# Kernel tuning notes

Hardware: AMD Instinct MI355X
Metric: run time of the kernel (lower is better)

Reference implementation:

```python
import jax, jax.numpy as jnp
import numpy as np

B, S, D = 4, 1024, 512
E = 16            # num_skills
DH = 4 * D        # expert hidden
DS = 2 * D        # shared expert hidden
TOP_K = 2
TEMP = 0.7
SHARED_SCALE = 0.25
EPS = 1e-5

def layer_norm(x, g, b):
    mu = jnp.mean(x, axis=-1, keepdims=True)
    var = jnp.mean(jnp.square(x - mu), axis=-1, keepdims=True)
    return (x - mu) * jax.lax.rsqrt(var + EPS) * g + b

def setup_inputs() -> dict:
    key = jax.random.key(0)
    ks = jax.random.split(key, 12)
    s = 0.02
    return {
        "x": jax.random.normal(ks[0], (B, S, D), jnp.float32),
        # input LayerNorm
        "ln_in_g": jnp.ones((D,), jnp.float32),
        "ln_in_b": jnp.zeros((D,), jnp.float32),
        # router Linear(D -> E)
        "router_w": jax.random.normal(ks[1], (D, E), jnp.float32) * s,
        "router_b": jnp.zeros((E,), jnp.float32),
        # experts: Linear(D->DH), SiLU, Linear(DH->D), stacked over E
        "ew1": jax.random.normal(ks[2], (E, D, DH), jnp.float32) * s,
        "eb1": jnp.zeros((E, DH), jnp.float32),
        "ew2": jax.random.normal(ks[3], (E, DH, D), jnp.float32) * s,
        "eb2": jnp.zeros((E, D), jnp.float32),
        # shared expert: Linear(D->DS), SiLU, Linear(DS->D), *0.25
        "sw1": jax.random.normal(ks[4], (D, DS), jnp.float32) * s,
        "sb1": jnp.zeros((DS,), jnp.float32),
        "sw2": jax.random.normal(ks[5], (DS, D), jnp.float32) * s,
        "sb2": jnp.zeros((D,), jnp.float32),
        # final ff: LayerNorm, Linear(D->4D), SiLU, Linear(4D->D)
        "ff_ln_g": jnp.ones((D,), jnp.float32),
        "ff_ln_b": jnp.zeros((D,), jnp.float32),
        "ff_w1": jax.random.normal(ks[6], (D, DH), jnp.float32) * s,
        "ff_b1": jnp.zeros((DH,), jnp.float32),
        "ff_w2": jax.random.normal(ks[7], (DH, D), jnp.float32) * s,
        "ff_b2": jnp.zeros((D,), jnp.float32),
    }

def reference(x, ln_in_g, ln_in_b, router_w, router_b,
              ew1, eb1, ew2, eb2, sw1, sb1, sw2, sb2,
              ff_ln_g, ff_ln_b, ff_w1, ff_b1, ff_w2, ff_b2):
    h = layer_norm(x, ln_in_g, ln_in_b)                      # [B,S,D]
    # router: softmax(Linear(h)/temperature)
    gate = jax.nn.softmax((h @ router_w + router_b) / TEMP, axis=-1)  # [B,S,E]
    vals, idx = jax.lax.top_k(gate, TOP_K)                   # [B,S,K]
    # combine weights per expert: sum_j vals_j * onehot(idx_j)
    comb = jnp.sum(jax.nn.one_hot(idx, E, dtype=h.dtype) * vals[..., None], axis=-2)  # [B,S,E]
    # all-expert forward (same math as masked loop in the original)
    eh = jax.nn.silu(jnp.einsum('bsd,edh->ebsh', h, ew1) + eb1[:, None, None, :])      # [E,B,S,DH]
    ey = jnp.einsum('ebsh,ehd->ebsd', eh, ew2) + eb2[:, None, None, :]                  # [E,B,S,D]
    mix = jnp.einsum('bse,ebsd->bsd', comb, ey)              # top-k weighted combine
    shared = (jax.nn.silu(h @ sw1 + sb1) @ sw2 + sb2) * SHARED_SCALE
    moe_out = mix + shared                                   # h after MoE
    fh = layer_norm(moe_out, ff_ln_g, ff_ln_b)
    ff_out = jax.nn.silu(fh @ ff_w1 + ff_b1) @ ff_w2 + ff_b2
    return x + moe_out + ff_out
```

## Files before the change

### kernel.cpp

```cpp
#include <hip/hip_runtime.h>
#include <stdint.h>

#define T_TOK 4096
#define DIM   512
#define NEXP  16
#define DHID  2048
#define DSH   1024
#define ROWSCAP 10240
#define MAXTILES 80

typedef __bf16 bf16x8 __attribute__((ext_vector_type(8)));
typedef float  f32x4  __attribute__((ext_vector_type(4)));
typedef unsigned short usv8 __attribute__((ext_vector_type(8)));

__device__ __forceinline__ unsigned short f2b(float f) {
  union { float f; unsigned int u; } un; un.f = f;
  unsigned int u = un.u + 0x7fffu + ((un.u >> 16) & 1u);
  return (unsigned short)(u >> 16);
}
__device__ __forceinline__ float b2f(unsigned short u) {
  union { unsigned int u; float f; } un; un.u = ((unsigned int)u) << 16; return un.f;
}

__device__ __forceinline__ void async16(void* lds, const void* gp) {
  __builtin_amdgcn_global_load_lds(
      (const __attribute__((address_space(1))) unsigned int*)gp,
      (__attribute__((address_space(3))) unsigned int*)lds, 16, 0, 0);
}

__device__ __forceinline__ void transpose64(
    const float* __restrict__ s, unsigned short* __restrict__ d, int R, int C,
    int tx, int ty, unsigned short* tile) {
  const int tid = threadIdx.x;
  const int c0 = tx * 64, r0 = ty * 64;
  const int r = tid >> 4, j = tid & 15;
#pragma unroll
  for (int p = 0; p < 4; ++p) {
    const int row = r + p * 16;
    const float4 v = *(const float4*)&s[(size_t)(r0 + row) * C + c0 + j * 4];
    tile[(j * 4 + 0) * 72 + row] = f2b(v.x);
    tile[(j * 4 + 1) * 72 + row] = f2b(v.y);
    tile[(j * 4 + 2) * 72 + row] = f2b(v.z);
    tile[(j * 4 + 3) * 72 + row] = f2b(v.w);
  }
  __syncthreads();
  const int jj = tid & 7, cc = tid >> 3;
#pragma unroll
  for (int p = 0; p < 2; ++p) {
    const int c = cc + p * 32;
    const usv8 u = *(const usv8*)&tile[c * 72 + jj * 8];
    *(usv8*)&d[(size_t)(c0 + c) * R + r0 + jj * 8] = u;
  }
}

__global__ __launch_bounds__(256) void prep_kernel(
    const float* __restrict__ x, const float* __restrict__ g, const float* __restrict__ b,
    const float* __restrict__ rw, const float* __restrict__ rb,
    unsigned short* __restrict__ hbuf, int* __restrict__ comb_idx, float* __restrict__ comb_w,
    int* __restrict__ counts,
    const float* __restrict__ ew1, const float* __restrict__ ew2,
    const float* __restrict__ sw1, const float* __restrict__ sw2,
    const float* __restrict__ fw1, const float* __restrict__ fw2,
    unsigned short* __restrict__ ew1T, unsigned short* __restrict__ ew2T,
    unsigned short* __restrict__ sw1T, unsigned short* __restrict__ sw2T,
    unsigned short* __restrict__ fw1T, unsigned short* __restrict__ fw2T) {
  __shared__ unsigned short tile[64 * 72];
  __shared__ int hist[NEXP];
  const int id = blockIdx.x;
  if (id >= 1024) {
    int id2 = id - 1024;
    const float* s; unsigned short* d; int R, C, t, tx, ty;
    if (id2 < 4096)      { int bm = id2 >> 8; t = id2 & 255; R = 512;  C = 2048;
                           s = ew1 + (size_t)bm * R * C; d = ew1T + (size_t)bm * R * C;
                           tx = t & 31; ty = t >> 5; }
    else if (id2 < 8192) { id2 -= 4096; int bm = id2 >> 8; t = id2 & 255; R = 2048; C = 512;
                           s = ew2 + (size_t)bm * R * C; d = ew2T + (size_t)bm * R * C;
                           tx = t & 7;  ty = t >> 3; }
    else if (id2 < 8320) { t = id2 - 8192; R = 512;  C = 1024; s = sw1; d = sw1T; tx = t & 15; ty = t >> 4; }
    else if (id2 < 8448) { t = id2 - 8320; R = 1024; C = 512;  s = sw2; d = sw2T; tx = t & 7;  ty = t >> 3; }
    else if (id2 < 8704) { t = id2 - 8448; R = 512;  C = 2048; s = fw1; d = fw1T; tx = t & 31; ty = t >> 5; }
    else                 { t = id2 - 8704; R = 2048; C = 512;  s = fw2; d = fw2T; tx = t & 7;  ty = t >> 3; }
    transpose64(s, d, R, C, tx, ty, tile);
    return;
  }
  const int wid = threadIdx.x >> 6, lane = threadIdx.x & 63;
  const int t = id * 4 + wid;
  if (threadIdx.x < NEXP) hist[threadIdx.x] = 0;
  __syncthreads();

  const float4* xr = (const float4*)(x + (size_t)t * DIM);
  const float4 va = xr[lane], vb = xr[lane + 64];
  float s = (va.x + va.y) + (va.z + va.w) + ((vb.x + vb.y) + (vb.z + vb.w));
#pragma unroll
  for (int o = 32; o; o >>= 1) s += __shfl_xor(s, o, 64);
  const float mu = s * (1.f / DIM);
  float da[4] = {va.x - mu, va.y - mu, va.z - mu, va.w - mu};
  float db[4] = {vb.x - mu, vb.y - mu, vb.z - mu, vb.w - mu};
  float q = (da[0]*da[0] + da[1]*da[1]) + (da[2]*da[2] + da[3]*da[3]) +
            ((db[0]*db[0] + db[1]*db[1]) + (db[2]*db[2] + db[3]*db[3]));
#pragma unroll
  for (int o = 32; o; o >>= 1) q += __shfl_xor(q, o, 64);
  const float rs = rsqrtf(q * (1.f / DIM) + 1e-5f);
  const float4 ga = ((const float4*)g)[lane], gb4 = ((const float4*)g)[lane + 64];
  const float4 ba = ((const float4*)b)[lane], bb4 = ((const float4*)b)[lane + 64];
  float ha[4], hbv[4];
  ha[0] = da[0] * rs * ga.x + ba.x;  ha[1] = da[1] * rs * ga.y + ba.y;
  ha[2] = da[2] * rs * ga.z + ba.z;  ha[3] = da[3] * rs * ga.w + ba.w;
  hbv[0] = db[0] * rs * gb4.x + bb4.x;  hbv[1] = db[1] * rs * gb4.y + bb4.y;
  hbv[2] = db[2] * rs * gb4.z + bb4.z;  hbv[3] = db[3] * rs * gb4.w + bb4.w;
  ushort4 ua = {f2b(ha[0]), f2b(ha[1]), f2b(ha[2]), f2b(ha[3])};
  ushort4 ub = {f2b(hbv[0]), f2b(hbv[1]), f2b(hbv[2]), f2b(hbv[3])};
  ((ushort4*)(hbuf + (size_t)t * DIM))[lane] = ua;
  ((ushort4*)(hbuf + (size_t)t * DIM))[lane + 64] = ub;

  float p[NEXP];
#pragma unroll
  for (int e = 0; e < NEXP; ++e) p[e] = 0.f;
  const int col0 = lane * 4;
#pragma unroll
  for (int half = 0; half < 2; ++half) {
#pragma unroll
    for (int j = 0; j < 4; ++j) {
      const int col = half * 256 + col0 + j;
      const float hv = half ? hbv[j] : ha[j];
      const float4* wr = (const float4*)(rw + (size_t)col * NEXP);
#pragma unroll
      for (int qq = 0; qq < 4; ++qq) {
        const float4 w = wr[qq];
        p[qq * 4 + 0] += hv * w.x;  p[qq * 4 + 1] += hv * w.y;
        p[qq * 4 + 2] += hv * w.z;  p[qq * 4 + 3] += hv * w.w;
      }
    }
  }
#pragma unroll
  for (int o = 32; o; o >>= 1) {
#pragma unroll
    for (int e = 0; e < NEXP; ++e) p[e] += __shfl_xor(p[e], o, 64);
  }
  float mx = -1e30f;
#pragma unroll
  for (int e = 0; e < NEXP; ++e) {
    p[e] = (p[e] + rb[e]) * (1.f / 0.7f);
    mx = fmaxf(mx, p[e]);
  }
  float ge[NEXP], se = 0.f;
#pragma unroll
  for (int e = 0; e < NEXP; ++e) { ge[e] = __expf(p[e] - mx); se += ge[e]; }
  const float inv = 1.f / se;
  int i0 = 0; float m0 = ge[0];
#pragma unroll
  for (int e = 1; e < NEXP; ++e) if (ge[e] > m0) { m0 = ge[e]; i0 = e; }
  int i1 = -1; float m1 = -1.f;
#pragma unroll
  for (int e = 0; e < NEXP; ++e) if (e != i0 && ge[e] > m1) { m1 = ge[e]; i1 = e; }
  if (lane == 0) {
    comb_idx[t * 2] = i0; comb_idx[t * 2 + 1] = i1;
    comb_w[t * 2] = m0 * inv; comb_w[t * 2 + 1] = m1 * inv;
    atomicAdd(&hist[i0], 1); atomicAdd(&hist[i1], 1);
  }
  __syncthreads();
  if (threadIdx.x < NEXP) {
    const int c = hist[threadIdx.x];
    if (c) atomicAdd(&counts[threadIdx.x], c);
  }
}

__global__ void plan_kernel(const int* __restrict__ counts, int* __restrict__ offs,
                            int* __restrict__ fill, int* __restrict__ tiledesc) {
  if (threadIdx.x == 0) {
    int run = 0, tix = 0;
    for (int e = 0; e < NEXP; ++e) {
      offs[e] = run;
      const int nt = (counts[e] + 127) >> 7;
      for (int i = 0; i < nt; ++i) { tiledesc[tix * 2] = e; tiledesc[tix * 2 + 1] = run + i * 128; ++tix; }
      run += nt * 128;
    }
    for (; tix < MAXTILES; ++tix) { tiledesc[tix * 2] = -1; tiledesc[tix * 2 + 1] = 0; }
  }
  if (threadIdx.x < NEXP) fill[threadIdx.x] = 0;
}

__global__ __launch_bounds__(256) void scatter_kernel(
    const int* __restrict__ comb_idx, const float* __restrict__ comb_w,
    const int* __restrict__ offs, int* __restrict__ fill,
    int* __restrict__ token_list, int* __restrict__ slots) {
  const int t = blockIdx.x * 256 + threadIdx.x;
#pragma unroll
  for (int j = 0; j < 2; ++j) {
    const int e = comb_idx[t * 2 + j];
    const int p = atomicAdd(&fill[e], 1);
    const int gidx = offs[e] + p;
    token_list[gidx] = t;
    slots[t * 2 + j] = gidx;
  }
}

__global__ __launch_bounds__(256) void combine_ln_kernel(
    const unsigned short* __restrict__ eyb, const float* __restrict__ shb,
    const int* __restrict__ slots, const float* __restrict__ comb_w,
    const float* __restrict__ g, const float* __restrict__ b,
    float* __restrict__ moe, unsigned short* __restrict__ fhb) {
  const int wid = threadIdx.x >> 6, lane = threadIdx.x & 63;
  const int t = blockIdx.x * 4 + wid;
  const int s0 = slots[t * 2], s1 = slots[t * 2 + 1];
  const float w0 = comb_w[t * 2], w1 = comb_w[t * 2 + 1];
  const uint4 E0 = ((const uint4*)(eyb + (size_t)s0 * DIM))[lane];
  const uint4 E1 = ((const uint4*)(eyb + (size_t)s1 * DIM))[lane];
  const float4 sa = ((const float4*)(shb + (size_t)t * DIM))[lane * 2];
  const float4 sb = ((const float4*)(shb + (size_t)t * DIM))[lane * 2 + 1];
  const unsigned int e0[4] = {E0.x, E0.y, E0.z, E0.w};
  const unsigned int e1[4] = {E1.x, E1.y, E1.z, E1.w};
  const float shv[8] = {sa.x, sa.y, sa.z, sa.w, sb.x, sb.y, sb.z, sb.w};
  float m[8];
#pragma unroll
  for (int j = 0; j < 4; ++j) {
    m[2*j]   = w0 * b2f((unsigned short)(e0[j] & 0xffff)) + w1 * b2f((unsigned short)(e1[j] & 0xffff)) + shv[2*j];
    m[2*j+1] = w0 * b2f((unsigned short)(e0[j] >> 16))    + w1 * b2f((unsigned short)(e1[j] >> 16))    + shv[2*j+1];
  }
  float4* mo = (float4*)(moe + (size_t)t * DIM);
  mo[lane * 2]     = make_float4(m[0], m[1], m[2], m[3]);
  mo[lane * 2 + 1] = make_float4(m[4], m[5], m[6], m[7]);
  float s = 0.f;
#pragma unroll
  for (int j = 0; j < 8; ++j) s += m[j];
#pragma unroll
  for (int o = 32; o; o >>= 1) s += __shfl_xor(s, o, 64);
  const float mu = s * (1.f / DIM);
  float q = 0.f;
#pragma unroll
  for (int j = 0; j < 8; ++j) { const float d = m[j] - mu; q += d * d; }
#pragma unroll
  for (int o = 32; o; o >>= 1) q += __shfl_xor(q, o, 64);
  const float rs = rsqrtf(q * (1.f / DIM) + 1e-5f);
  const float4 ga = ((const float4*)g)[lane * 2], gb4 = ((const float4*)g)[lane * 2 + 1];
  const float4 ba = ((const float4*)b)[lane * 2], bb4 = ((const float4*)b)[lane * 2 + 1];
  const float gv[8] = {ga.x, ga.y, ga.z, ga.w, gb4.x, gb4.y, gb4.z, gb4.w};
  const float bv[8] = {ba.x, ba.y, ba.z, ba.w, bb4.x, bb4.y, bb4.z, bb4.w};
  ushort4 o0, o1;
  o0.x = f2b((m[0]-mu)*rs*gv[0]+bv[0]); o0.y = f2b((m[1]-mu)*rs*gv[1]+bv[1]);
  o0.z = f2b((m[2]-mu)*rs*gv[2]+bv[2]); o0.w = f2b((m[3]-mu)*rs*gv[3]+bv[3]);
  o1.x = f2b((m[4]-mu)*rs*gv[4]+bv[4]); o1.y = f2b((m[5]-mu)*rs*gv[5]+bv[5]);
  o1.z = f2b((m[6]-mu)*rs*gv[6]+bv[6]); o1.w = f2b((m[7]-mu)*rs*gv[7]+bv[7]);
  ((ushort4*)(fhb + (size_t)t * DIM))[lane * 2]     = o0;
  ((ushort4*)(fhb + (size_t)t * DIM))[lane * 2 + 1] = o1;
}

template <int MODE, bool EXPERT>
__device__ __forceinline__ void gemm_body(
    const unsigned short* __restrict__ A, int lda,
    const unsigned short* __restrict__ BT, const float* __restrict__ bias,
    int K, int N, int row0, int expert, int bn,
    const int* __restrict__ token_list,
    unsigned short* __restrict__ outA, const float* __restrict__ mix,
    const float* __restrict__ xres, float* __restrict__ outp,
    unsigned short* As, unsigned short* Bs) {
  const int tid = threadIdx.x;
  const unsigned short* Bt = BT + (size_t)expert * N * K + (size_t)bn * 128 * K;
  const float* bp = bias + (EXPERT ? expert * N : 0) + bn * 128;

  const int r_a = tid >> 2;
  const int c8 = ((((tid & 3) - (tid >> 3)) & 3)) << 3;
  const unsigned short* arow0; const unsigned short* arow1;
  if (EXPERT && MODE == 0) {
    int t0 = token_list[row0 + r_a];       if (t0 < 0) t0 = 0;
    int t1 = token_list[row0 + r_a + 64];  if (t1 < 0) t1 = 0;
    arow0 = A + (size_t)t0 * lda + c8;
    arow1 = A + (size_t)t1 * lda + c8;
  } else {
    arow0 = A + (size_t)(row0 + r_a) * lda + c8;
    arow1 = A + (size_t)(row0 + r_a + 64) * lda + c8;
  }
  const unsigned short* brow0 = Bt + (size_t)r_a * K + c8;
  const unsigned short* brow1 = Bt + (size_t)(r_a + 64) * K + c8;

  const int lane = tid & 63, wid = tid >> 6;
  const int wm = wid & 1, wn = wid >> 1;
  const int l15 = lane & 15, qd = lane >> 4;

  char* asb0 = (char*)As + wid * 1024;
  char* asb1 = (char*)As + 4096 + wid * 1024;
  char* bsb0 = (char*)Bs + wid * 1024;
  char* bsb1 = (char*)Bs + 4096 + wid * 1024;

  f32x4 acc[4][4] = {};
  const int rdsw = ((qd + (l15 >> 1)) & 3) * 8;
  const bf16x8* afp = (const bf16x8*)&As[(wm * 64 + l15) * 32 + rdsw];
  const bf16x8* bfp = (const bf16x8*)&Bs[(wn * 64 + l15) * 32 + rdsw];

  for (int k0 = 0; k0 < K; k0 += 32) {
    __syncthreads();
    async16(asb0, arow0 + k0);
    async16(asb1, arow1 + k0);
    async16(bsb0, brow0 + k0);
    async16(bsb1, brow1 + k0);
    __syncthreads();
    bf16x8 af[4], bq[4];
#pragma unroll
    for (int a = 0; a < 4; ++a) af[a] = afp[a * 64];
#pragma unroll
    for (int b2 = 0; b2 < 4; ++b2) bq[b2] = bfp[b2 * 64];
#pragma unroll
    for (int a = 0; a < 4; ++a)
#pragma unroll
      for (int b2 = 0; b2 < 4; ++b2)
        acc[a][b2] = __builtin_amdgcn_mfma_f32_16x16x32_bf16(af[a], bq[b2], acc[a][b2], 0, 0, 0);
  }

  const int mloc = wm * 64 + qd * 4;
  const int nloc = wn * 64 + l15;
#pragma unroll
  for (int b2 = 0; b2 < 4; ++b2) {
    const int n = bn * 128 + nloc + b2 * 16;
    const float bv = bp[nloc + b2 * 16];
#pragma unroll
    for (int a = 0; a < 4; ++a) {
#pragma unroll
      for (int r = 0; r < 4; ++r) {
        const int m = mloc + a * 16 + r;
        const float val = acc[a][b2][r] + bv;
        if (MODE == 0) {
          const float sg = val / (1.f + __expf(-val));
          outA[(size_t)(row0 + m) * N + n] = f2b(sg);
        } else if (MODE == 1) {
          outA[(size_t)(row0 + m) * N + n] = f2b(val);
        } else if (MODE == 2) {
          outp[(size_t)(row0 + m) * DIM + n] = 0.25f * val;
        } else {
          const size_t o = (size_t)(row0 + m) * DIM + n;
          outp[o] = xres[o] + mix[o] + val;
        }
      }
    }
  }
}

__global__ __launch_bounds__(256) void gemm_g1(
    const unsigned short* __restrict__ hb,
    const unsigned short* __restrict__ ew1T, const float* __restrict__ eb1,
    const unsigned short* __restrict__ sw1T, const float* __restrict__ sb1,
    const int* __restrict__ tiledesc, const int* __restrict__ token_list,
    unsigned short* __restrict__ Abuf, unsigned short* __restrict__ Sbuf) {
  __shared__ unsigned short As[128 * 32];
  __shared__ unsigned short Bs[128 * 32];
  const int id = blockIdx.x;
  if (id < MAXTILES * 16) {
    const int by = id >> 4, bn = id & 15;
    const int expert = tiledesc[by * 2];
    if (expert < 0) return;
    const int row0 = tiledesc[by * 2 + 1];
    gemm_body<0, true>(hb, DIM, ew1T, eb1, DIM, DHID, row0, expert, bn,
                       token_list, Abuf, nullptr, nullptr, nullptr, As, Bs);
  } else {
    const int id2 = id - MAXTILES * 16;
    const int by = id2 >> 3, bn = id2 & 7;
    gemm_body<0, false>(hb, DIM, sw1T, sb1, DIM, DSH, by * 128, 0, bn,
                        nullptr, Sbuf, nullptr, nullptr, nullptr, As, Bs);
  }
}

__global__ __launch_bounds__(256) void gemm_g2(
    const unsigned short* __restrict__ Abuf,
    const unsigned short* __restrict__ ew2T, const float* __restrict__ eb2,
    const unsigned short* __restrict__ Sbuf,
    const unsigned short* __restrict__ sw2T, const float* __restrict__ sb2,
    const int* __restrict__ tiledesc,
    unsigned short* __restrict__ eyb, float* __restrict__ shb) {
  __shared__ unsigned short As[128 * 32];
  __shared__ unsigned short Bs[128 * 32];
  const int id = blockIdx.x;
  if (id < MAXTILES * 4) {
    const int by = id >> 2, bn = id & 3;
    const int expert = tiledesc[by * 2];
    if (expert < 0) return;
    const int row0 = tiledesc[by * 2 + 1];
    gemm_body<1, true>(Abuf, DHID, ew2T, eb2, DHID, DIM, row0, expert, bn,
                       nullptr, eyb, nullptr, nullptr, nullptr, As, Bs);
  } else {
    const int id2 = id - MAXTILES * 4;
    const int by = id2 >> 2, bn = id2 & 3;
    gemm_body<2, false>(Sbuf, DSH, sw2T, sb2, DSH, DIM, by * 128, 0, bn,
                        nullptr, nullptr, nullptr, nullptr, shb, As, Bs);
  }
}

template <int MODE>
__global__ __launch_bounds__(256) void gemm_kernel(
    const unsigned short* __restrict__ A, int lda,
    const unsigned short* __restrict__ BT, const float* __restrict__ bias, int K, int N,
    unsigned short* __restrict__ outA, const float* __restrict__ mix,
    const float* __restrict__ xres, float* __restrict__ outp) {
  __shared__ unsigned short As[128 * 32];
  __shared__ unsigned short Bs[128 * 32];
  gemm_body<MODE, false>(A, lda, BT, bias, K, N, blockIdx.y * 128, 0, blockIdx.x,
                         nullptr, outA, mix, xres, outp, As, Bs);
}

extern "C" void kernel_launch(void* const* d_in, const int* in_sizes, int n_in,
                              void* d_out, int out_size, void* d_ws, size_t ws_size,
                              hipStream_t stream) {
  (void)in_sizes; (void)n_in; (void)out_size; (void)ws_size;
  const float* x    = (const float*)d_in[0];
  const float* lng  = (const float*)d_in[1];
  const float* lnb  = (const float*)d_in[2];
  const float* rw   = (const float*)d_in[3];
  const float* rb   = (const float*)d_in[4];
  const float* ew1  = (const float*)d_in[5];
  const float* eb1  = (const float*)d_in[6];
  const float* ew2  = (const float*)d_in[7];
  const float* eb2  = (const float*)d_in[8];
  const float* sw1  = (const float*)d_in[9];
  const float* sb1  = (const float*)d_in[10];
  const float* sw2  = (const float*)d_in[11];
  const float* sb2  = (const float*)d_in[12];
  const float* flng = (const float*)d_in[13];
  const float* flnb = (const float*)d_in[14];
  const float* fw1  = (const float*)d_in[15];
  const float* fb1  = (const float*)d_in[16];
  const float* fw2  = (const float*)d_in[17];
  const float* fb2  = (const float*)d_in[18];
  float* out = (float*)d_out;

  char* ws = (char*)d_ws;
  size_t off = 0;
  auto alloc = [&](size_t bytes) -> void* {
    void* p = ws + off;
    off += (bytes + 255) & ~(size_t)255;
    return p;
  };
  unsigned short* ew1T = (unsigned short*)alloc((size_t)NEXP * DIM * DHID * 2);
  unsigned short* ew2T = (unsigned short*)alloc((size_t)NEXP * DHID * DIM * 2);
  unsigned short* sw1T = (unsigned short*)alloc((size_t)DIM * DSH * 2);
  unsigned short* sw2T = (unsigned short*)alloc((size_t)DSH * DIM * 2);
  unsigned short* fw1T = (unsigned short*)alloc((size_t)DIM * DHID * 2);
  unsigned short* fw2T = (unsigned short*)alloc((size_t)DHID * DIM * 2);
  unsigned short* hb   = (unsigned short*)alloc((size_t)T_TOK * DIM * 2);
  unsigned short* fhb  = (unsigned short*)alloc((size_t)T_TOK * DIM * 2);
  unsigned short* Abuf = (unsigned short*)alloc((size_t)ROWSCAP * DHID * 2);
  unsigned short* Sbuf = (unsigned short*)alloc((size_t)T_TOK * DSH * 2);
  unsigned short* eyb  = (unsigned short*)alloc((size_t)ROWSCAP * DIM * 2);
  float* shb = (float*)alloc((size_t)T_TOK * DIM * 4);
  float* moe = (float*)alloc((size_t)T_TOK * DIM * 4);
  int*   comb_idx = (int*)alloc((size_t)T_TOK * 2 * 4);
  float* comb_w   = (float*)alloc((size_t)T_TOK * 2 * 4);
  int*   slots    = (int*)alloc((size_t)T_TOK * 2 * 4);
  int* counts   = (int*)alloc(64);
  int* offs     = (int*)alloc(64);
  int* fill     = (int*)alloc(64);
  int* tiledesc = (int*)alloc(MAXTILES * 2 * 4);
  int* token_list = (int*)alloc((size_t)ROWSCAP * 4);

  hipMemsetAsync(counts, 0, 64, stream);
  hipMemsetAsync(token_list, 0xFF, (size_t)ROWSCAP * 4, stream);

  prep_kernel<<<9984, 256, 0, stream>>>(x, lng, lnb, rw, rb, hb, comb_idx, comb_w, counts,
                                        ew1, ew2, sw1, sw2, fw1, fw2,
                                        ew1T, ew2T, sw1T, sw2T, fw1T, fw2T);
  plan_kernel<<<1, 64, 0, stream>>>(counts, offs, fill, tiledesc);
  scatter_kernel<<<T_TOK / 256, 256, 0, stream>>>(comb_idx, comb_w, offs, fill, token_list, slots);

  gemm_g1<<<MAXTILES * 16 + 256, 256, 0, stream>>>(hb, ew1T, eb1, sw1T, sb1,
                                                   tiledesc, token_list, Abuf, Sbuf);
  gemm_g2<<<MAXTILES * 4 + 128, 256, 0, stream>>>(Abuf, ew2T, eb2, Sbuf, sw2T, sb2,
                                                  tiledesc, eyb, shb);
  combine_ln_kernel<<<T_TOK / 4, 256, 0, stream>>>(eyb, shb, slots, comb_w, flng, flnb, moe, fhb);
  gemm_kernel<0><<<dim3(DHID / 128, T_TOK / 128), 256, 0, stream>>>(
      fhb, DIM, fw1T, fb1, DIM, DHID, Abuf, nullptr, nullptr, nullptr);
  gemm_kernel<3><<<dim3(DIM / 128, T_TOK / 128), 256, 0, stream>>>(
      Abuf, DHID, fw2T, fb2, DHID, DIM, nullptr, moe, x, out);
}
```

Before: 436.6 us.

## Use 64-row tiles for down-projection GEMMs and fp32 LDS transpose

Templates the GEMM body on row-tile height and runs the expert/shared down-projections and the final FF2 GEMM with 64-row tiles. This doubles the block count for these N=512 GEMMs so more CUs are busy. The cost is lower per-block data reuse, since each B tile is reloaded twice as often. Separately, the weight transpose now stores fp32 into a padded LDS tile and converts to bf16 on the read side, aiming to cut LDS bank conflicts from scattered 16-bit writes.

```diff
diff --git a/kernel.cpp b/kernel.cpp
--- a/kernel.cpp
+++ b/kernel.cpp
@@ -30,25 +30,27 @@
 
 __device__ __forceinline__ void transpose64(
     const float* __restrict__ s, unsigned short* __restrict__ d, int R, int C,
-    int tx, int ty, unsigned short* tile) {
+    int tx, int ty, float* tile) {
   const int tid = threadIdx.x;
   const int c0 = tx * 64, r0 = ty * 64;
-  const int r = tid >> 4, j = tid & 15;
+  const int r = tid >> 4, j4 = (tid & 15) * 4;
 #pragma unroll
   for (int p = 0; p < 4; ++p) {
     const int row = r + p * 16;
-    const float4 v = *(const float4*)&s[(size_t)(r0 + row) * C + c0 + j * 4];
-    tile[(j * 4 + 0) * 72 + row] = f2b(v.x);
-    tile[(j * 4 + 1) * 72 + row] = f2b(v.y);
-    tile[(j * 4 + 2) * 72 + row] = f2b(v.z);
-    tile[(j * 4 + 3) * 72 + row] = f2b(v.w);
+    const float4 v = *(const float4*)&s[(size_t)(r0 + row) * C + c0 + j4];
+    tile[row * 65 + j4 + 0] = v.x;
+    tile[row * 65 + j4 + 1] = v.y;
+    tile[row * 65 + j4 + 2] = v.z;
+    tile[row * 65 + j4 + 3] = v.w;
   }
   __syncthreads();
   const int jj = tid & 7, cc = tid >> 3;
 #pragma unroll
   for (int p = 0; p < 2; ++p) {
     const int c = cc + p * 32;
-    const usv8 u = *(const usv8*)&tile[c * 72 + jj * 8];
+    usv8 u;
+#pragma unroll
+    for (int i = 0; i < 8; ++i) u[i] = f2b(tile[(jj * 8 + i) * 65 + c]);
     *(usv8*)&d[(size_t)(c0 + c) * R + r0 + jj * 8] = u;
   }
 }
@@ -64,7 +66,7 @@
     unsigned short* __restrict__ ew1T, unsigned short* __restrict__ ew2T,
     unsigned short* __restrict__ sw1T, unsigned short* __restrict__ sw2T,
     unsigned short* __restrict__ fw1T, unsigned short* __restrict__ fw2T) {
-  __shared__ unsigned short tile[64 * 72];
+  __shared__ float tile[64 * 65];
   __shared__ int hist[NEXP];
   const int id = blockIdx.x;
   if (id >= 1024) {
@@ -245,7 +247,7 @@
   ((ushort4*)(fhb + (size_t)t * DIM))[lane * 2 + 1] = o1;
 }
 
-template <int MODE, bool EXPERT>
+template <int MODE, bool EXPERT, int BM>
 __device__ __forceinline__ void gemm_body(
     const unsigned short* __restrict__ A, int lda,
     const unsigned short* __restrict__ BT, const float* __restrict__ bias,
@@ -258,17 +260,20 @@
   const unsigned short* Bt = BT + (size_t)expert * N * K + (size_t)bn * 128 * K;
   const float* bp = bias + (EXPERT ? expert * N : 0) + bn * 128;
 
+  const int MA = BM / 64;
   const int r_a = tid >> 2;
   const int c8 = ((((tid & 3) - (tid >> 3)) & 3)) << 3;
-  const unsigned short* arow0; const unsigned short* arow1;
+  const unsigned short* arow0; const unsigned short* arow1 = nullptr;
   if (EXPERT && MODE == 0) {
     int t0 = token_list[row0 + r_a];       if (t0 < 0) t0 = 0;
-    int t1 = token_list[row0 + r_a + 64];  if (t1 < 0) t1 = 0;
     arow0 = A + (size_t)t0 * lda + c8;
-    arow1 = A + (size_t)t1 * lda + c8;
+    if (MA == 2) {
+      int t1 = token_list[row0 + r_a + 64];  if (t1 < 0) t1 = 0;
+      arow1 = A + (size_t)t1 * lda + c8;
+    }
   } else {
     arow0 = A + (size_t)(row0 + r_a) * lda + c8;
-    arow1 = A + (size_t)(row0 + r_a + 64) * lda + c8;
+    if (MA == 2) arow1 = A + (size_t)(row0 + r_a + 64) * lda + c8;
   }
   const unsigned short* brow0 = Bt + (size_t)r_a * K + c8;
   const unsigned short* brow1 = Bt + (size_t)(r_a + 64) * K + c8;
@@ -276,44 +281,46 @@
   const int lane = tid & 63, wid = tid >> 6;
   const int wm = wid & 1, wn = wid >> 1;
   const int l15 = lane & 15, qd = lane >> 4;
+  const int WR = BM / 2;
+  const int NA = WR / 16;
 
   char* asb0 = (char*)As + wid * 1024;
   char* asb1 = (char*)As + 4096 + wid * 1024;
   char* bsb0 = (char*)Bs + wid * 1024;
   char* bsb1 = (char*)Bs + 4096 + wid * 1024;
 
-  f32x4 acc[4][4] = {};
+  f32x4 acc[NA][4] = {};
   const int rdsw = ((qd + (l15 >> 1)) & 3) * 8;
-  const bf16x8* afp = (const bf16x8*)&As[(wm * 64 + l15) * 32 + rdsw];
+  const bf16x8* afp = (const bf16x8*)&As[(wm * WR + l15) * 32 + rdsw];
   const bf16x8* bfp = (const bf16x8*)&Bs[(wn * 64 + l15) * 32 + rdsw];
 
   for (int k0 = 0; k0 < K; k0 += 32) {
     __syncthreads();
     async16(asb0, arow0 + k0);
-    async16(asb1, arow1 + k0);
+    if (MA == 2) async16(asb1, arow1 + k0);
     async16(bsb0, brow0 + k0);
     async16(bsb1, brow1 + k0);
     __syncthreads();
-    bf16x8 af[4], bq[4];
-#pragma unroll
-    for (int a = 0; a < 4; ++a) af[a] = afp[a * 64];
+    bf16x8 af[NA], bq[4];
+#pragma unroll
+    for (int a = 0; a < NA; ++a) af[a] = afp[a * 64];
 #pragma unroll
     for (int b2 = 0; b2 < 4; ++b2) bq[b2] = bfp[b2 * 64];
 #pragma unroll
-    for (int a = 0; a < 4; ++a)
+    for (int a = 0; a < NA; ++a)
 #pragma unroll
       for (int b2 = 0; b2 < 4; ++b2)
         acc[a][b2] = __builtin_amdgcn_mfma_f32_16x16x32_bf16(af[a], bq[b2], acc[a][b2], 0, 0, 0);
   }
 
-  const int mloc = wm * 64 + qd * 4;
+  const int mloc = wm * WR + qd * 4;
   const int nloc = wn * 64 + l15;
 #pragma unroll
   for (int b2 = 0; b2 < 4; ++b2) {
     const int n = bn * 128 + nloc + b2 * 16;
     const float bv = bp[nloc + b2 * 16];
 #pragma unroll
-    for (int a = 0; a < 4; ++a) {
+    for (int a = 0; a < NA; ++a) {
 #pragma unroll
       for (int r = 0; r < 4; ++r) {
         const int m = mloc + a * 16 + r;
@@ -348,13 +355,13 @@
     const int expert = tiledesc[by * 2];
     if (expert < 0) return;
     const int row0 = tiledesc[by * 2 + 1];
-    gemm_body<0, true>(hb, DIM, ew1T, eb1, DIM, DHID, row0, expert, bn,
-                       token_list, Abuf, nullptr, nullptr, nullptr, As, Bs);
+    gemm_body<0, true, 128>(hb, DIM, ew1T, eb1, DIM, DHID, row0, expert, bn,
+                            token_list, Abuf, nullptr, nullptr, nullptr, As, Bs);
   } else {
     const int id2 = id - MAXTILES * 16;
     const int by = id2 >> 3, bn = id2 & 7;
-    gemm_body<0, false>(hb, DIM, sw1T, sb1, DIM, DSH, by * 128, 0, bn,
-                        nullptr, Sbuf, nullptr, nullptr, nullptr, As, Bs);
+    gemm_body<0, false, 128>(hb, DIM, sw1T, sb1, DIM, DSH, by * 128, 0, bn,
+                             nullptr, Sbuf, nullptr, nullptr, nullptr, As, Bs);
   }
 }
 
@@ -365,34 +372,42 @@
     const unsigned short* __restrict__ sw2T, const float* __restrict__ sb2,
     const int* __restrict__ tiledesc,
     unsigned short* __restrict__ eyb, float* __restrict__ shb) {
+  __shared__ unsigned short As[64 * 32];
+  __shared__ unsigned short Bs[128 * 32];
+  const int id = blockIdx.x;
+  if (id < MAXTILES * 8) {
+    const int seg = id >> 3, sub = (id >> 2) & 1, bn = id & 3;
+    const int expert = tiledesc[seg * 2];
+    if (expert < 0) return;
+    const int row0 = tiledesc[seg * 2 + 1] + sub * 64;
+    gemm_body<1, true, 64>(Abuf, DHID, ew2T, eb2, DHID, DIM, row0, expert, bn,
+                           nullptr, eyb, nullptr, nullptr, nullptr, As, Bs);
+  } else {
+    const int id2 = id - MAXTILES * 8;
+    const int by = id2 >> 2, bn = id2 & 3;
+    gemm_body<2, false, 64>(Sbuf, DSH, sw2T, sb2, DSH, DIM, by * 64, 0, bn,
+                            nullptr, nullptr, nullptr, nullptr, shb, As, Bs);
+  }
+}
+
+__global__ __launch_bounds__(256) void gemm_ff1(
+    const unsigned short* __restrict__ A,
+    const unsigned short* __restrict__ BT, const float* __restrict__ bias,
+    unsigned short* __restrict__ outA) {
   __shared__ unsigned short As[128 * 32];
   __shared__ unsigned short Bs[128 * 32];
-  const int id = blockIdx.x;
-  if (id < MAXTILES * 4) {
-    const int by = id >> 2, bn = id & 3;
-    const int expert = tiledesc[by * 2];
-    if (expert < 0) return;
-    const int row0 = tiledesc[by * 2 + 1];
-    gemm_body<1, true>(Abuf, DHID, ew2T, eb2, DHID, DIM, row0, expert, bn,
-                       nullptr, eyb, nullptr, nullptr, nullptr, As, Bs);
-  } else {
-    const int id2 = id - MAXTILES * 4;
-    const int by = id2 >> 2, bn = id2 & 3;
-    gemm_body<2, false>(Sbuf, DSH, sw2T, sb2, DSH, DIM, by * 128, 0, bn,
-                        nullptr, nullptr, nullptr, nullptr, shb, As, Bs);
-  }
-}
-
-template <int MODE>
-__global__ __launch_bounds__(256) void gemm_kernel(
-    const unsigned short* __restrict__ A, int lda,
-    const unsigned short* __restrict__ BT, const float* __restrict__ bias, int K, int N,
-    unsigned short* __restrict__ outA, const float* __restrict__ mix,
-    const float* __restrict__ xres, float* __restrict__ outp) {
-  __shared__ unsigned short As[128 * 32];
+  gemm_body<0, false, 128>(A, DIM, BT, bias, DIM, DHID, blockIdx.y * 128, 0, blockIdx.x,
+                           nullptr, outA, nullptr, nullptr, nullptr, As, Bs);
+}
+__global__ __launch_bounds__(256) void gemm_ff2(
+    const unsigned short* __restrict__ A,
+    const unsigned short* __restrict__ BT, const float* __restrict__ bias,
+    const float* __restrict__ mix, const float* __restrict__ xres,
+    float* __restrict__ outp) {
+  __shared__ unsigned short As[64 * 32];
   __shared__ unsigned short Bs[128 * 32];
-  gemm_body<MODE, false>(A, lda, BT, bias, K, N, blockIdx.y * 128, 0, blockIdx.x,
-                         nullptr, outA, mix, xres, outp, As, Bs);
+  gemm_body<3, false, 64>(A, DHID, BT, bias, DHID, DIM, blockIdx.y * 64, 0, blockIdx.x,
+                          nullptr, nullptr, mix, xres, outp, As, Bs);
 }
 
 extern "C" void kernel_launch(void* const* d_in, const int* in_sizes, int n_in,
@@ -460,11 +475,9 @@
 
   gemm_g1<<<MAXTILES * 16 + 256, 256, 0, stream>>>(hb, ew1T, eb1, sw1T, sb1,
                                                    tiledesc, token_list, Abuf, Sbuf);
-  gemm_g2<<<MAXTILES * 4 + 128, 256, 0, stream>>>(Abuf, ew2T, eb2, Sbuf, sw2T, sb2,
+  gemm_g2<<<MAXTILES * 8 + 256, 256, 0, stream>>>(Abuf, ew2T, eb2, Sbuf, sw2T, sb2,
                                                   tiledesc, eyb, shb);
   combine_ln_kernel<<<T_TOK / 4, 256, 0, stream>>>(eyb, shb, slots, comb_w, flng, flnb, moe, fhb);
-  gemm_kernel<0><<<dim3(DHID / 128, T_TOK / 128), 256, 0, stream>>>(
-      fhb, DIM, fw1T, fb1, DIM, DHID, Abuf, nullptr, nullptr, nullptr);
-  gemm_kernel<3><<<dim3(DIM / 128, T_TOK / 128), 256, 0, stream>>>(
-      Abuf, DHID, fw2T, fb2, DHID, DIM, nullptr, moe, x, out);
-}
+  gemm_ff1<<<dim3(DHID / 128, T_TOK / 128), 256, 0, stream>>>(fhb, fw1T, fb1, Abuf);
+  gemm_ff2<<<dim3(DIM / 128, T_TOK / 64), 256, 0, stream>>>(Abuf, fw2T, fb2, moe, x, out);
+}
```

New measurement: 400.7 us. 1.09x faster.
